# Kernel tuning notes

Measured on AMD Instinct MI355X. Metric: run time of the kernel, lower is better.

Reference implementation:

```python
import jax, jax.numpy as jnp
import numpy as np

B, N, E, H, DIN, DB, P, L, NB = 2, 10000, 100000, 128, 8, 16, 3, 2, 3


def setup_inputs() -> dict:
    key = jax.random.key(0)
    ks = jax.random.split(key, 16)

    def rn(i, shape, s=0.05):
        return jax.random.normal(ks[i], shape, dtype=jnp.float32) * s

    return {
        "x": jax.random.normal(ks[0], (B, DIN), dtype=jnp.float32),
        "base_features": rn(1, (N, DB), 1.0),
        "base_positions": rn(2, (N, P), 1.0),
        "Win": rn(3, (DB + DIN, H)),
        "b_in": jnp.zeros((H,), jnp.float32),
        "msg_W1": rn(4, (L, NB, 2 * H + 1, H)),
        "msg_b1": jnp.zeros((L, NB, H), jnp.float32),
        "msg_W2": rn(5, (L, NB, H, H)),
        "msg_b2": jnp.zeros((L, NB, H), jnp.float32),
        "pos_W1": rn(6, (L, NB, H, H)),
        "pos_b1": jnp.zeros((L, NB, H), jnp.float32),
        "pos_W2": rn(7, (L, NB, H, 1)),
        "pos_b2": jnp.zeros((L, NB, 1), jnp.float32),
        "upd_W1": rn(8, (L, 2 * H, H)),
        "upd_b1": jnp.zeros((L, H), jnp.float32),
        "upd_W2": rn(9, (L, H, H)),
        "upd_b2": jnp.zeros((L, H), jnp.float32),
        "out_W1": rn(10, (H, H)),
        "out_b1": jnp.zeros((H,), jnp.float32),
        "out_W2": rn(11, (H, 1)),
        "out_b2": jnp.zeros((1,), jnp.float32),
        "entity_indices": jax.random.randint(ks[12], (B,), 0, N),
        "edge_src": jax.random.randint(ks[13], (NB, E), 0, N),
        "edge_dst": jax.random.randint(ks[14], (NB, E), 0, N),
    }


def reference(x, base_features, base_positions, Win, b_in,
              msg_W1, msg_b1, msg_W2, msg_b2,
              pos_W1, pos_b1, pos_W2, pos_b2,
              upd_W1, upd_b1, upd_W2, upd_b2,
              out_W1, out_b1, out_W2, out_b2,
              entity_indices, edge_src, edge_dst):
    silu = jax.nn.silu
    b = x.shape[0]
    n = base_features.shape[0]
    # scatter each batch element's dynamic features onto its entity cell
    dynamic = jnp.zeros((b, n, x.shape[1]), x.dtype).at[jnp.arange(b), entity_indices].set(x)
    base = jnp.broadcast_to(base_features[None], (b, n, base_features.shape[1]))
    h = jnp.concatenate([base, dynamic], axis=-1) @ Win + b_in          # [B,N,H]
    p = jnp.broadcast_to(base_positions[None], (b, n, base_positions.shape[1]))  # [B,N,3]
    n_layers, n_nbhd = msg_W1.shape[0], edge_src.shape[0]
    for l in range(n_layers):
        m_sum = jnp.zeros_like(h)
        p_new = p
        for k in range(n_nbhd):
            src, dst = edge_src[k], edge_dst[k]
            # degree of aggregation target (matches torch bincount over indices[1])
            deg = jnp.clip(jnp.zeros((n,), h.dtype).at[dst].add(1.0), 1.0)[None, :, None]
            rel = p[:, dst] - p[:, src]                                  # [B,E,3]
            d2 = jnp.sum(rel * rel, axis=-1, keepdims=True)              # [B,E,1]
            m = silu(jnp.concatenate([h[:, dst], h[:, src], d2], axis=-1) @ msg_W1[l, k] + msg_b1[l, k])
            m = silu(m @ msg_W2[l, k] + msg_b2[l, k])                    # [B,E,H]
            m_sum = m_sum + jnp.zeros_like(h).at[:, dst].add(m) / deg
            coef = silu(m @ pos_W1[l, k] + pos_b1[l, k]) @ pos_W2[l, k] + pos_b2[l, k]  # [B,E,1]
            p_new = p_new + jnp.zeros_like(p).at[:, dst].add(rel * coef) / deg
        h = h + (silu(jnp.concatenate([h, m_sum], axis=-1) @ upd_W1[l] + upd_b1[l]) @ upd_W2[l] + upd_b2[l])
        p = p_new
    e = h[jnp.arange(b), entity_indices]                                 # [B,H] gather readout
    return silu(e @ out_W1 + out_b1) @ out_W2 + out_b2                   # [B,1]
```

## Files before the change

kernel.cpp:

```cpp
#include <hip/hip_runtime.h>
#include <hip/hip_bf16.h>
#include <math.h>

#define Bc   2
#define Nc   10000
#define Ec   100000
#define Hc   128
#define DINc 8
#define DBc  16
#define NBc  3
#define Lc   2
#define EB   3125

typedef float v4 __attribute__((ext_vector_type(4)));
typedef float f32x16 __attribute__((ext_vector_type(16)));
typedef _Float16 h8 __attribute__((ext_vector_type(8)));
typedef _Float16 h4 __attribute__((ext_vector_type(4)));

__device__ __forceinline__ float silu_f(float x) {
  return x * __builtin_amdgcn_rcpf(1.f + __expf(-x));
}

__device__ __forceinline__ h4 pack4(float a, float b, float c, float d) {
  typedef decltype(__builtin_amdgcn_cvt_pkrtz(0.f, 0.f)) pk2;
  union { h4 v; pk2 p[2]; } u;
  u.p[0] = __builtin_amdgcn_cvt_pkrtz(a, b);
  u.p[1] = __builtin_amdgcn_cvt_pkrtz(c, d);
  return u.v;
}


__global__ void zero4_kernel(float* __restrict__ p, int n4) {
  int i = blockIdx.x * blockDim.x + threadIdx.x;
  if (i < n4) ((v4*)p)[i] = (v4)(0.f);
}

__global__ void copy_kernel(float* __restrict__ dst, const float* __restrict__ src, int n) {
  int i = blockIdx.x * blockDim.x + threadIdx.x;
  if (i < n) dst[i] = src[i];
}


__global__ void hist_kernel(int* __restrict__ hist, const int* __restrict__ edst) {
  int i = blockIdx.x * blockDim.x + threadIdx.x;
  if (i < NBc * Ec) {
    int k = i / Ec;
    atomicAdd(&hist[k * Nc + edst[i]], 1);
  }
}

__global__ void scan_kernel(const int* __restrict__ hist, int* __restrict__ offs,
                            float* __restrict__ deginv) {
  const int k = blockIdx.x, tid = threadIdx.x;
  const int NPT = 40;
  __shared__ int part[256];
  int local[NPT];
  int sum = 0;
  for (int j = 0; j < NPT; ++j) {
    int n = tid * NPT + j;
    if (n < Nc) { local[j] = sum; sum += hist[k * Nc + n]; }
  }
  part[tid] = sum;
  __syncthreads();
  for (int off = 1; off < 256; off <<= 1) {
    int v = (tid >= off) ? part[tid - off] : 0;
    __syncthreads();
    part[tid] += v;
    __syncthreads();
  }
  int excl = part[tid] - sum;
  for (int j = 0; j < NPT; ++j) {
    int n = tid * NPT + j;
    if (n < Nc) {
      offs[k * Nc + n] = excl + local[j];
      deginv[k * Nc + n] = 1.f / fmaxf((float)hist[k * Nc + n], 1.f);
    }
  }
}

__global__ void sort_scatter_kernel(int* __restrict__ sorted, int* __restrict__ cursor,
                                    const int* __restrict__ offs, const int* __restrict__ edst) {
  int i = blockIdx.x * blockDim.x + threadIdx.x;
  if (i < NBc * Ec) {
    int k = i / Ec, e = i - k * Ec;
    int d = edst[i];
    int pos = offs[k * Nc + d] + atomicAdd(&cursor[k * Nc + d], 1);
    sorted[k * Ec + pos] = e;
  }
}


__global__ void init_h_kernel(_Float16* __restrict__ h16, const float* __restrict__ bfeat,
                              const float* __restrict__ x, const float* __restrict__ Win,
                              const float* __restrict__ b_in, const int* __restrict__ ent) {
  int g = blockIdx.x * blockDim.x + threadIdx.x;
  if (g >= Bc * Nc * Hc) return;
  int j = g & (Hc - 1);
  int bn = g >> 7;
  int n = bn % Nc;
  int b = bn / Nc;
  float acc = b_in[j];
#pragma unroll
  for (int i = 0; i < DBc; ++i) acc = fmaf(bfeat[n * DBc + i], Win[i * Hc + j], acc);
  if (n == ent[b]) {
#pragma unroll
    for (int i = 0; i < DINc; ++i) acc = fmaf(x[b * DINc + i], Win[(DBc + i) * Hc + j], acc);
  }
  h16[g] = (_Float16)acc;
}

__global__ void init_p_kernel(float* __restrict__ p, const float* __restrict__ bp) {
  int i = blockIdx.x * blockDim.x + threadIdx.x;
  if (i < Bc * Nc * 3) p[i] = bp[i % (Nc * 3)];
}

__global__ void conv_ext_kernel(_Float16* __restrict__ dst, const float* __restrict__ src,
                                const float* __restrict__ bias,
                                int nchunk, int total, int realRows, int biasRow) {
  int g = blockIdx.x * blockDim.x + threadIdx.x;
  if (g >= total) return;
  int j = g & 7;
  int lane = (g >> 3) & 63;
  int q = g >> 9;
  int t = q % nchunk;
  int q2 = q / nchunk;
  int wave = q2 & 3;
  int mat = q2 >> 2;
  int kk = t * 16 + (lane >> 5) * 8 + j;
  int col = (wave << 5) + (lane & 31);
  float v = 0.f;
  if (kk < realRows)      v = src[((size_t)mat * realRows + kk) * Hc + col];
  else if (kk == biasRow) v = bias[mat * Hc + col];
  dst[g] = (_Float16)v;
}


__global__ __launch_bounds__(256, 8)
void edge_mfma_kernel(const _Float16* __restrict__ h16, const float* __restrict__ p,
                      float* __restrict__ m_sum, float* __restrict__ p_new,
                      const float* __restrict__ deginv,
                      const int* __restrict__ esrc, const int* __restrict__ edst,
                      const int* __restrict__ sorted,
                      const _Float16* __restrict__ W1e, const _Float16* __restrict__ W2e,
                      const _Float16* __restrict__ P1e,
                      const float* __restrict__ pW2, const float* __restrict__ pb2,
                      int l) {
  const int k = blockIdx.y, lk = l * NBc + k;
  const int b = (blockIdx.x >= EB) ? 1 : 0;
  const int pos0 = (blockIdx.x - b * EB) << 5;
  const int tid = threadIdx.x;
  const int wave = tid >> 6, lane = tid & 63;
  const int lrow = lane & 31, lhalf = lane >> 5;

  __shared__ __align__(16) _Float16 RegA[16 * 512];
  __shared__ __align__(16) _Float16 Dchk[512];
  __shared__ int shd[32], shs[32], sdi[32];
  __shared__ float sdinvs[32], srel[32][3], scoef[32];
  __shared__ float cpw2[Hc];
  __shared__ unsigned sflush;

  if (tid < Hc) cpw2[tid] = pW2[lk * Hc + tid];
  if (tid < 32) {
    int e = sorted[k * Ec + pos0 + tid];
    int si = esrc[k * Ec + e], di = edst[k * Ec + e];
    int nd = b * Nc + di, ns = b * Nc + si;
    const float* pd = &p[(size_t)nd * 3];
    const float* ps = &p[(size_t)ns * 3];
    float rx = pd[0] - ps[0], ry = pd[1] - ps[1], rz = pd[2] - ps[2];
    srel[tid][0] = rx; srel[tid][1] = ry; srel[tid][2] = rz;
    float d2 = rx * rx + ry * ry + rz * rz;
    sdinvs[tid] = deginv[k * Nc + di];
    sdi[tid] = di;
    shd[tid] = nd * Hc; shs[tid] = ns * Hc;
    scoef[tid] = 0.f;
    h8 dv = (h8)(_Float16)0.f;
    dv[0] = (_Float16)d2; dv[1] = (_Float16)1.f;
    *(h8*)&Dchk[tid * 8] = dv;
    int prev = __shfl_up(di, 1);
    bool isStart = (tid == 0) || (di != prev);
    unsigned long long m = __ballot(isStart);
    if (tid == 0) sflush = (unsigned)((m >> 1) | 0x80000000ull);
  } else if (tid < 64) {
    h8 dv = (h8)(_Float16)0.f;
    *(h8*)&Dchk[tid * 8] = dv;
  }
  __syncthreads();

  {
    const int i = tid & 31, c = tid >> 5;
    h8 v0 = *(const h8*)&h16[shd[i] + c * 8];
    h8 v1 = *(const h8*)&h16[shd[i] + 64 + c * 8];
    h8 v2 = *(const h8*)&h16[shs[i] + c * 8];
    h8 v3 = *(const h8*)&h16[shs[i] + 64 + c * 8];
    int slot = (i + ((c & 1) << 5)) << 3;
    int tb = (c >> 1) << 9;
    *(h8*)&RegA[tb + 0 * 2048 + slot] = v0;
    *(h8*)&RegA[tb + 4 * 512  + slot] = v1;
    *(h8*)&RegA[tb + 8 * 512  + slot] = v2;
    *(h8*)&RegA[tb + 12 * 512 + slot] = v3;
  }
  __syncthreads();

  const _Float16* wb1 = &W1e[(size_t)(lk * 4 + wave) * (17 * 512)];
  f32x16 acc;
#pragma unroll
  for (int r = 0; r < 16; ++r) acc[r] = 0.f;
#pragma unroll
  for (int t = 0; t < 16; ++t) {
    h8 bact = *(const h8*)&RegA[t * 512 + lane * 8];
    h8 aw   = *(const h8*)&wb1[t * 512 + lane * 8];
    acc = __builtin_amdgcn_mfma_f32_32x32x16_f16(aw, bact, acc, 0, 0, 0);
  }
  {
    h8 bact = *(const h8*)&Dchk[lane * 8];
    h8 aw   = *(const h8*)&wb1[16 * 512 + lane * 8];
    acc = __builtin_amdgcn_mfma_f32_32x32x16_f16(aw, bact, acc, 0, 0, 0);
  }
  h4 m1pk[4];
#pragma unroll
  for (int c = 0; c < 4; ++c)
    m1pk[c] = pack4(silu_f(acc[c * 4 + 0]), silu_f(acc[c * 4 + 1]),
                    silu_f(acc[c * 4 + 2]), silu_f(acc[c * 4 + 3]));
  __syncthreads();
#pragma unroll
  for (int c = 0; c < 4; ++c) {
    int t = (wave << 1) + (c >> 1);
    int slot = lrow + ((c & 1) << 5);
    *(h4*)&RegA[t * 512 + slot * 8 + lhalf * 4] = m1pk[c];
  }
  __syncthreads();

  const _Float16* wb2 = &W2e[(size_t)(lk * 4 + wave) * (9 * 512)];
  f32x16 acc2;
#pragma unroll
  for (int r = 0; r < 16; ++r) acc2[r] = 0.f;
#pragma unroll
  for (int t = 0; t < 8; ++t) {
    h8 bact = *(const h8*)&RegA[t * 512 + lane * 8];
    h8 aw   = *(const h8*)&wb2[t * 512 + lane * 8];
    acc2 = __builtin_amdgcn_mfma_f32_32x32x16_f16(aw, bact, acc2, 0, 0, 0);
  }
  {
    h8 bact = *(const h8*)&Dchk[lane * 8];
    h8 aw   = *(const h8*)&wb2[8 * 512 + lane * 8];
    acc2 = __builtin_amdgcn_mfma_f32_32x32x16_f16(aw, bact, acc2, 0, 0, 0);
  }
  h4 m2pk[4];
#pragma unroll
  for (int c = 0; c < 4; ++c) {
    m2pk[c] = pack4(silu_f(acc2[c * 4 + 0]), silu_f(acc2[c * 4 + 1]),
                    silu_f(acc2[c * 4 + 2]), silu_f(acc2[c * 4 + 3]));
    int t = 8 + (wave << 1) + (c >> 1);
    int slot = lrow + ((c & 1) << 5);
    *(h4*)&RegA[t * 512 + slot * 8 + lhalf * 4] = m2pk[c];
  }
  __syncthreads();
  {
    char* rm = (char*)RegA;
#pragma unroll
    for (int c = 0; c < 4; ++c) {
      int hb = (wave << 5) + (c << 3) + (lhalf << 2);
      *(h4*)(rm + (lrow << 8) + (((hb << 1)) ^ ((lrow & 15) << 4))) = m2pk[c];
    }
  }

  const _Float16* wb3 = &P1e[(size_t)(lk * 4 + wave) * (9 * 512)];
  f32x16 acc3;
#pragma unroll
  for (int r = 0; r < 16; ++r) acc3[r] = 0.f;
#pragma unroll
  for (int t = 0; t < 8; ++t) {
    h8 bact = *(const h8*)&RegA[(8 + t) * 512 + lane * 8];
    h8 aw   = *(const h8*)&wb3[t * 512 + lane * 8];
    acc3 = __builtin_amdgcn_mfma_f32_32x32x16_f16(aw, bact, acc3, 0, 0, 0);
  }
  {
    h8 bact = *(const h8*)&Dchk[lane * 8];
    h8 aw   = *(const h8*)&wb3[8 * 512 + lane * 8];
    acc3 = __builtin_amdgcn_mfma_f32_32x32x16_f16(aw, bact, acc3, 0, 0, 0);
  }
  {
    float csum = 0.f;
#pragma unroll
    for (int r = 0; r < 16; ++r) {
      int hg = (wave << 5) + (r & 3) + ((r >> 2) << 3) + (lhalf << 2);
      csum += silu_f(acc3[r]) * cpw2[hg];
    }
    csum += __shfl_down(csum, 32);
    if (lane < 32) atomicAdd(&scoef[lrow], csum);
  }
  __syncthreads();

  {
    const int col = tid & 127;
    const int r0 = (tid >> 7) << 4;
    const size_t bbase = (size_t)b * Nc * Hc;
    const unsigned fm = sflush;
    const char* rm = (const char*)RegA;
    float accv = 0.f;
#pragma unroll
    for (int rr = 0; rr < 16; ++rr) {
      int r = r0 + rr;
      float v = (float)*(const _Float16*)(rm + (r << 8) + (((col << 1)) ^ ((r & 15) << 4)));
      accv += v;
      if ((fm >> r) & 1u) {
        atomicAdd(&m_sum[bbase + (size_t)sdi[r] * Hc + col], accv * sdinvs[r]);
        accv = 0.f;
      }
    }
    if (r0 == 0 && !((fm >> 15) & 1u))
      atomicAdd(&m_sum[bbase + (size_t)sdi[15] * Hc + col], accv * sdinvs[15]);
  }
  if (tid < 32) {
    float cf = (scoef[tid] + pb2[lk]) * sdinvs[tid];
    float* pp = &p_new[((size_t)(b * Nc + sdi[tid])) * 3];
    atomicAdd(&pp[0], srel[tid][0] * cf);
    atomicAdd(&pp[1], srel[tid][1] * cf);
    atomicAdd(&pp[2], srel[tid][2] * cf);
  }
}


__global__ __launch_bounds__(256, 8)
void update_mfma_kernel(_Float16* __restrict__ h16, const float* __restrict__ m_sum,
                        const _Float16* __restrict__ U1e, const _Float16* __restrict__ U2e,
                        int l) {
  const int tid = threadIdx.x;
  const int wave = tid >> 6, lane = tid & 63;
  const int lrow = lane & 31, lhalf = lane >> 5;
  const int row0 = blockIdx.x << 5;

  __shared__ __align__(16) _Float16 RegA[16 * 512];
  __shared__ __align__(16) _Float16 Dchk[512];

  if (tid < 64) {
    h8 dv = (h8)(_Float16)0.f;
    if (tid < 32) dv[1] = (_Float16)1.f;
    *(h8*)&Dchk[tid * 8] = dv;
  }
  {
    const int i = tid & 31, c = tid >> 5;
    size_t hb = (size_t)(row0 + i) * Hc;
    h8 v0 = *(const h8*)&h16[hb + c * 8];
    h8 v1 = *(const h8*)&h16[hb + 64 + c * 8];
    v4 m0 = *(const v4*)&m_sum[hb + c * 8];
    v4 m1 = *(const v4*)&m_sum[hb + c * 8 + 4];
    v4 m2 = *(const v4*)&m_sum[hb + 64 + c * 8];
    v4 m3 = *(const v4*)&m_sum[hb + 64 + c * 8 + 4];
    union { h8 v; h4 q[2]; } w0, w1;
    w0.q[0] = pack4(m0[0], m0[1], m0[2], m0[3]);
    w0.q[1] = pack4(m1[0], m1[1], m1[2], m1[3]);
    w1.q[0] = pack4(m2[0], m2[1], m2[2], m2[3]);
    w1.q[1] = pack4(m3[0], m3[1], m3[2], m3[3]);
    int slot = (i + ((c & 1) << 5)) << 3;
    int tb = (c >> 1) << 9;
    *(h8*)&RegA[tb + slot] = v0;
    *(h8*)&RegA[tb + 4 * 512 + slot] = v1;
    *(h8*)&RegA[tb + 8 * 512 + slot] = w0.v;
    *(h8*)&RegA[tb + 12 * 512 + slot] = w1.v;
  }
  __syncthreads();

  const _Float16* wb1 = &U1e[(size_t)(l * 4 + wave) * (17 * 512)];
  f32x16 acc;
#pragma unroll
  for (int r = 0; r < 16; ++r) acc[r] = 0.f;
#pragma unroll
  for (int t = 0; t < 16; ++t) {
    h8 bact = *(const h8*)&RegA[t * 512 + lane * 8];
    h8 aw   = *(const h8*)&wb1[t * 512 + lane * 8];
    acc = __builtin_amdgcn_mfma_f32_32x32x16_f16(aw, bact, acc, 0, 0, 0);
  }
  {
    h8 bact = *(const h8*)&Dchk[lane * 8];
    h8 aw   = *(const h8*)&wb1[16 * 512 + lane * 8];
    acc = __builtin_amdgcn_mfma_f32_32x32x16_f16(aw, bact, acc, 0, 0, 0);
  }
  h4 u1pk[4];
#pragma unroll
  for (int c = 0; c < 4; ++c)
    u1pk[c] = pack4(silu_f(acc[c * 4 + 0]), silu_f(acc[c * 4 + 1]),
                    silu_f(acc[c * 4 + 2]), silu_f(acc[c * 4 + 3]));
  __syncthreads();
#pragma unroll
  for (int c = 0; c < 4; ++c) {
    int t = (wave << 1) + (c >> 1);
    int slot = lrow + ((c & 1) << 5);
    *(h4*)&RegA[t * 512 + slot * 8 + lhalf * 4] = u1pk[c];
  }
  __syncthreads();

  const _Float16* wb2 = &U2e[(size_t)(l * 4 + wave) * (9 * 512)];
  f32x16 acc2;
#pragma unroll
  for (int r = 0; r < 16; ++r) acc2[r] = 0.f;
#pragma unroll
  for (int t = 0; t < 8; ++t) {
    h8 bact = *(const h8*)&RegA[t * 512 + lane * 8];
    h8 aw   = *(const h8*)&wb2[t * 512 + lane * 8];
    acc2 = __builtin_amdgcn_mfma_f32_32x32x16_f16(aw, bact, acc2, 0, 0, 0);
  }
  {
    h8 bact = *(const h8*)&Dchk[lane * 8];
    h8 aw   = *(const h8*)&wb2[8 * 512 + lane * 8];
    acc2 = __builtin_amdgcn_mfma_f32_32x32x16_f16(aw, bact, acc2, 0, 0, 0);
  }
  {
    _Float16* hp = &h16[(size_t)(row0 + lrow) * Hc];
#pragma unroll
    for (int c = 0; c < 4; ++c) {
      int hb = (wave << 5) + (c << 3) + (lhalf << 2);
      h4 old = *(const h4*)&hp[hb];
      *(h4*)&hp[hb] = pack4((float)old[0] + acc2[c * 4 + 0], (float)old[1] + acc2[c * 4 + 1],
                            (float)old[2] + acc2[c * 4 + 2], (float)old[3] + acc2[c * 4 + 3]);
    }
  }
}


__global__ void readout_kernel(const _Float16* __restrict__ h16, const int* __restrict__ ent,
                               const float* __restrict__ oW1, const float* __restrict__ ob1,
                               const float* __restrict__ oW2, const float* __restrict__ ob2,
                               float* __restrict__ out) {
  __shared__ float tb[Bc][Hc];
  int tid = threadIdx.x;
  int b = tid >> 7, j = tid & 127;
  const _Float16* e = &h16[((size_t)(b * Nc + ent[b])) * Hc];
  float a = ob1[j];
#pragma unroll 4
  for (int i = 0; i < Hc; ++i) a = fmaf((float)e[i], oW1[i * Hc + j], a);
  tb[b][j] = silu_f(a);
  __syncthreads();
  if (tid < Bc) {
    float s = ob2[0];
    for (int i = 0; i < Hc; ++i) s = fmaf(tb[tid][i], oW2[i], s);
    out[tid] = s;
  }
}


extern "C" void kernel_launch(void* const* d_in, const int* in_sizes, int n_in,
                              void* d_out, int out_size, void* d_ws, size_t ws_size,
                              hipStream_t stream) {
  const float* x    = (const float*)d_in[0];
  const float* bfe  = (const float*)d_in[1];
  const float* bp   = (const float*)d_in[2];
  const float* Win  = (const float*)d_in[3];
  const float* b_in = (const float*)d_in[4];
  const float* mW1  = (const float*)d_in[5];
  const float* mb1  = (const float*)d_in[6];
  const float* mW2  = (const float*)d_in[7];
  const float* mb2  = (const float*)d_in[8];
  const float* pW1  = (const float*)d_in[9];
  const float* pb1  = (const float*)d_in[10];
  const float* pW2  = (const float*)d_in[11];
  const float* pb2  = (const float*)d_in[12];
  const float* uW1  = (const float*)d_in[13];
  const float* ub1  = (const float*)d_in[14];
  const float* uW2  = (const float*)d_in[15];
  const float* ub2  = (const float*)d_in[16];
  const float* oW1  = (const float*)d_in[17];
  const float* ob1  = (const float*)d_in[18];
  const float* oW2  = (const float*)d_in[19];
  const float* ob2  = (const float*)d_in[20];
  const int* ent    = (const int*)d_in[21];
  const int* esrc   = (const int*)d_in[22];
  const int* edst   = (const int*)d_in[23];

  float* wsf = (float*)d_ws;
  float* msum   = wsf;  wsf += (size_t)Bc * Nc * Hc;
  float* pa     = wsf;  wsf += (size_t)Bc * Nc * 3;
  float* pb_    = wsf;  wsf += (size_t)Bc * Nc * 3;
  float* deginv = wsf;  wsf += (size_t)NBc * Nc;
  _Float16* h16 = (_Float16*)wsf;
  _Float16* W1e = h16 + (size_t)Bc * Nc * Hc;
  _Float16* W2e = W1e + 208896;
  _Float16* P1e = W2e + 110592;
  _Float16* U1e = P1e + 110592;
  _Float16* U2e = U1e + 69632;
  int* hist   = (int*)(U2e + 36864);
  int* cursor = hist + NBc * Nc;
  int* offs   = cursor + NBc * Nc;
  int* sorted = offs + NBc * Nc;

  zero4_kernel<<<dim3((2 * NBc * Nc / 4 + 255) / 256), dim3(256), 0, stream>>>((float*)hist, 2 * NBc * Nc / 4);
  hist_kernel<<<dim3((NBc * Ec + 255) / 256), dim3(256), 0, stream>>>(hist, edst);
  scan_kernel<<<dim3(NBc), dim3(256), 0, stream>>>(hist, offs, deginv);
  sort_scatter_kernel<<<dim3((NBc * Ec + 255) / 256), dim3(256), 0, stream>>>(sorted, cursor, offs, edst);

  conv_ext_kernel<<<dim3(816), dim3(256), 0, stream>>>(W1e, mW1, mb1, 17, 208896, 257, 257);
  conv_ext_kernel<<<dim3(432), dim3(256), 0, stream>>>(W2e, mW2, mb2, 9, 110592, 128, 129);
  conv_ext_kernel<<<dim3(432), dim3(256), 0, stream>>>(P1e, pW1, pb1, 9, 110592, 128, 129);
  conv_ext_kernel<<<dim3(272), dim3(256), 0, stream>>>(U1e, uW1, ub1, 17, 69632, 256, 257);
  conv_ext_kernel<<<dim3(144), dim3(256), 0, stream>>>(U2e, uW2, ub2, 9, 36864, 128, 129);

  init_h_kernel<<<dim3((Bc * Nc * Hc + 255) / 256), dim3(256), 0, stream>>>(h16, bfe, x, Win, b_in, ent);
  init_p_kernel<<<dim3((Bc * Nc * 3 + 255) / 256), dim3(256), 0, stream>>>(pa, bp);

  float* pcur = pa;
  float* pnew = pb_;
  const int nmh = Bc * Nc * Hc;
  for (int l = 0; l < Lc; ++l) {
    zero4_kernel<<<dim3((nmh / 4 + 255) / 256), dim3(256), 0, stream>>>(msum, nmh / 4);
    copy_kernel<<<dim3((Bc * Nc * 3 + 255) / 256), dim3(256), 0, stream>>>(pnew, pcur, Bc * Nc * 3);
    edge_mfma_kernel<<<dim3(Bc * EB, NBc), dim3(256), 0, stream>>>(
        h16, pcur, msum, pnew, deginv, esrc, edst, sorted,
        W1e, W2e, P1e, pW2, pb2, l);
    update_mfma_kernel<<<dim3(Bc * Nc / 32), dim3(256), 0, stream>>>(h16, msum, U1e, U2e, l);
    float* t = pcur; pcur = pnew; pnew = t;
  }
  readout_kernel<<<dim3(1), dim3(256), 0, stream>>>(h16, ent, oW1, ob1, oW2, ob2, (float*)d_out);
}
```

Before: 672.1 us.

## Process 64 edges per block, reusing each weight fragment across two MFMAs

The edge kernel now handles 64 sorted edges per block instead of 32, split into two 32-edge column groups that share each loaded weight fragment across two MFMA calls. This halves the weight reads from global memory per edge and halves the block count. The cost is double the LDS use and more registers per thread (launch bounds lowered to 4 blocks per CU). The m_sum scatter now reads the second-layer output straight from the regular tile layout instead of a separate swizzled copy, and flush detection uses a 64-bit mask keyed on the batch-offset node.

New measurement: 669.6 us. About the same (-0.4%).

```diff
diff --git a/kernel.cpp b/kernel.cpp
--- a/kernel.cpp
+++ b/kernel.cpp
@@ -10,7 +10,6 @@
 #define DBc  16
 #define NBc  3
 #define Lc   2
-#define EB   3125
 
 typedef float v4 __attribute__((ext_vector_type(4)));
 typedef float f32x16 __attribute__((ext_vector_type(16)));
@@ -135,7 +134,7 @@
 }
 
 
-__global__ __launch_bounds__(256, 8)
+__global__ __launch_bounds__(256, 4)
 void edge_mfma_kernel(const _Float16* __restrict__ h16, const float* __restrict__ p,
                       float* __restrict__ m_sum, float* __restrict__ p_new,
                       const float* __restrict__ deginv,
@@ -146,22 +145,22 @@
                       const float* __restrict__ pW2, const float* __restrict__ pb2,
                       int l) {
   const int k = blockIdx.y, lk = l * NBc + k;
-  const int b = (blockIdx.x >= EB) ? 1 : 0;
-  const int pos0 = (blockIdx.x - b * EB) << 5;
   const int tid = threadIdx.x;
   const int wave = tid >> 6, lane = tid & 63;
   const int lrow = lane & 31, lhalf = lane >> 5;
 
-  __shared__ __align__(16) _Float16 RegA[16 * 512];
-  __shared__ __align__(16) _Float16 Dchk[512];
-  __shared__ int shd[32], shs[32], sdi[32];
-  __shared__ float sdinvs[32], srel[32][3], scoef[32];
+  __shared__ __align__(16) _Float16 RegA[16384];
+  __shared__ __align__(16) _Float16 Dchk[1024];
+  __shared__ int shd[64], shs[64], sOff[64];
+  __shared__ float sdinv[64], srel[64][3], scoef[64];
   __shared__ float cpw2[Hc];
-  __shared__ unsigned sflush;
+  __shared__ unsigned long long sflush;
 
   if (tid < Hc) cpw2[tid] = pW2[lk * Hc + tid];
-  if (tid < 32) {
-    int e = sorted[k * Ec + pos0 + tid];
+  if (tid < 64) {
+    int pos = blockIdx.x * 64 + tid;
+    int b = (pos >= Ec) ? 1 : 0;
+    int e = sorted[k * Ec + (pos - b * Ec)];
     int si = esrc[k * Ec + e], di = edst[k * Ec + e];
     int nd = b * Nc + di, ns = b * Nc + si;
     const float* pd = &p[(size_t)nd * 3];
@@ -169,151 +168,163 @@
     float rx = pd[0] - ps[0], ry = pd[1] - ps[1], rz = pd[2] - ps[2];
     srel[tid][0] = rx; srel[tid][1] = ry; srel[tid][2] = rz;
     float d2 = rx * rx + ry * ry + rz * rz;
-    sdinvs[tid] = deginv[k * Nc + di];
-    sdi[tid] = di;
+    sdinv[tid] = deginv[k * Nc + di];
     shd[tid] = nd * Hc; shs[tid] = ns * Hc;
+    sOff[tid] = nd * Hc;
     scoef[tid] = 0.f;
     h8 dv = (h8)(_Float16)0.f;
+    h8 zv = (h8)(_Float16)0.f;
     dv[0] = (_Float16)d2; dv[1] = (_Float16)1.f;
-    *(h8*)&Dchk[tid * 8] = dv;
-    int prev = __shfl_up(di, 1);
-    bool isStart = (tid == 0) || (di != prev);
+    int g = tid >> 5, il = tid & 31;
+    *(h8*)&Dchk[g * 512 + il * 8] = dv;
+    *(h8*)&Dchk[g * 512 + 256 + il * 8] = zv;
+    int prevn = __shfl_up(nd, 1);
+    bool isStart = (tid == 0) || (nd != prevn);
     unsigned long long m = __ballot(isStart);
-    if (tid == 0) sflush = (unsigned)((m >> 1) | 0x80000000ull);
-  } else if (tid < 64) {
-    h8 dv = (h8)(_Float16)0.f;
-    *(h8*)&Dchk[tid * 8] = dv;
-  }
-  __syncthreads();
-
-  {
-    const int i = tid & 31, c = tid >> 5;
-    h8 v0 = *(const h8*)&h16[shd[i] + c * 8];
-    h8 v1 = *(const h8*)&h16[shd[i] + 64 + c * 8];
-    h8 v2 = *(const h8*)&h16[shs[i] + c * 8];
-    h8 v3 = *(const h8*)&h16[shs[i] + 64 + c * 8];
-    int slot = (i + ((c & 1) << 5)) << 3;
-    int tb = (c >> 1) << 9;
-    *(h8*)&RegA[tb + 0 * 2048 + slot] = v0;
-    *(h8*)&RegA[tb + 4 * 512  + slot] = v1;
-    *(h8*)&RegA[tb + 8 * 512  + slot] = v2;
-    *(h8*)&RegA[tb + 12 * 512 + slot] = v3;
+    if (tid == 0) sflush = (m >> 1) | (1ull << 63);
+  }
+  __syncthreads();
+
+  {
+    const int i = tid & 63, cg = tid >> 6;
+    const int g = i >> 5, il = i & 31;
+#pragma unroll
+    for (int q = 0; q < 4; ++q) {
+      int d0 = cg * 32 + q * 8;
+      int t = d0 >> 4;
+      int kh = q & 1;
+      h8 vd = *(const h8*)&h16[shd[i] + d0];
+      h8 vs = *(const h8*)&h16[shs[i] + d0];
+      *(h8*)&RegA[(t * 2 + g) * 512 + kh * 256 + il * 8] = vd;
+      *(h8*)&RegA[((8 + t) * 2 + g) * 512 + kh * 256 + il * 8] = vs;
+    }
   }
   __syncthreads();
 
   const _Float16* wb1 = &W1e[(size_t)(lk * 4 + wave) * (17 * 512)];
-  f32x16 acc;
-#pragma unroll
-  for (int r = 0; r < 16; ++r) acc[r] = 0.f;
+  f32x16 aA, aB;
+#pragma unroll
+  for (int r = 0; r < 16; ++r) { aA[r] = 0.f; aB[r] = 0.f; }
 #pragma unroll
   for (int t = 0; t < 16; ++t) {
-    h8 bact = *(const h8*)&RegA[t * 512 + lane * 8];
-    h8 aw   = *(const h8*)&wb1[t * 512 + lane * 8];
-    acc = __builtin_amdgcn_mfma_f32_32x32x16_f16(aw, bact, acc, 0, 0, 0);
-  }
-  {
-    h8 bact = *(const h8*)&Dchk[lane * 8];
-    h8 aw   = *(const h8*)&wb1[16 * 512 + lane * 8];
-    acc = __builtin_amdgcn_mfma_f32_32x32x16_f16(aw, bact, acc, 0, 0, 0);
-  }
-  h4 m1pk[4];
-#pragma unroll
-  for (int c = 0; c < 4; ++c)
-    m1pk[c] = pack4(silu_f(acc[c * 4 + 0]), silu_f(acc[c * 4 + 1]),
-                    silu_f(acc[c * 4 + 2]), silu_f(acc[c * 4 + 3]));
-  __syncthreads();
+    h8 aw = *(const h8*)&wb1[t * 512 + lane * 8];
+    h8 bA = *(const h8*)&RegA[(t * 2 + 0) * 512 + lane * 8];
+    h8 bB = *(const h8*)&RegA[(t * 2 + 1) * 512 + lane * 8];
+    aA = __builtin_amdgcn_mfma_f32_32x32x16_f16(aw, bA, aA, 0, 0, 0);
+    aB = __builtin_amdgcn_mfma_f32_32x32x16_f16(aw, bB, aB, 0, 0, 0);
+  }
+  {
+    h8 aw = *(const h8*)&wb1[16 * 512 + lane * 8];
+    h8 dA = *(const h8*)&Dchk[lane * 8];
+    h8 dB = *(const h8*)&Dchk[512 + lane * 8];
+    aA = __builtin_amdgcn_mfma_f32_32x32x16_f16(aw, dA, aA, 0, 0, 0);
+    aB = __builtin_amdgcn_mfma_f32_32x32x16_f16(aw, dB, aB, 0, 0, 0);
+  }
+  h4 m1A[4], m1B[4];
 #pragma unroll
   for (int c = 0; c < 4; ++c) {
-    int t = (wave << 1) + (c >> 1);
-    int slot = lrow + ((c & 1) << 5);
-    *(h4*)&RegA[t * 512 + slot * 8 + lhalf * 4] = m1pk[c];
+    m1A[c] = pack4(silu_f(aA[c * 4 + 0]), silu_f(aA[c * 4 + 1]),
+                   silu_f(aA[c * 4 + 2]), silu_f(aA[c * 4 + 3]));
+    m1B[c] = pack4(silu_f(aB[c * 4 + 0]), silu_f(aB[c * 4 + 1]),
+                   silu_f(aB[c * 4 + 2]), silu_f(aB[c * 4 + 3]));
+  }
+  __syncthreads();
+#pragma unroll
+  for (int c = 0; c < 4; ++c) {
+    int t = 2 * wave + (c >> 1);
+    int base = (c & 1) * 256 + lrow * 8 + lhalf * 4;
+    *(h4*)&RegA[(t * 2 + 0) * 512 + base] = m1A[c];
+    *(h4*)&RegA[(t * 2 + 1) * 512 + base] = m1B[c];
   }
   __syncthreads();
 
   const _Float16* wb2 = &W2e[(size_t)(lk * 4 + wave) * (9 * 512)];
-  f32x16 acc2;
-#pragma unroll
-  for (int r = 0; r < 16; ++r) acc2[r] = 0.f;
+#pragma unroll
+  for (int r = 0; r < 16; ++r) { aA[r] = 0.f; aB[r] = 0.f; }
 #pragma unroll
   for (int t = 0; t < 8; ++t) {
-    h8 bact = *(const h8*)&RegA[t * 512 + lane * 8];
-    h8 aw   = *(const h8*)&wb2[t * 512 + lane * 8];
-    acc2 = __builtin_amdgcn_mfma_f32_32x32x16_f16(aw, bact, acc2, 0, 0, 0);
-  }
-  {
-    h8 bact = *(const h8*)&Dchk[lane * 8];
-    h8 aw   = *(const h8*)&wb2[8 * 512 + lane * 8];
-    acc2 = __builtin_amdgcn_mfma_f32_32x32x16_f16(aw, bact, acc2, 0, 0, 0);
-  }
-  h4 m2pk[4];
+    h8 aw = *(const h8*)&wb2[t * 512 + lane * 8];
+    h8 bA = *(const h8*)&RegA[(t * 2 + 0) * 512 + lane * 8];
+    h8 bB = *(const h8*)&RegA[(t * 2 + 1) * 512 + lane * 8];
+    aA = __builtin_amdgcn_mfma_f32_32x32x16_f16(aw, bA, aA, 0, 0, 0);
+    aB = __builtin_amdgcn_mfma_f32_32x32x16_f16(aw, bB, aB, 0, 0, 0);
+  }
+  {
+    h8 aw = *(const h8*)&wb2[8 * 512 + lane * 8];
+    h8 dA = *(const h8*)&Dchk[lane * 8];
+    h8 dB = *(const h8*)&Dchk[512 + lane * 8];
+    aA = __builtin_amdgcn_mfma_f32_32x32x16_f16(aw, dA, aA, 0, 0, 0);
+    aB = __builtin_amdgcn_mfma_f32_32x32x16_f16(aw, dB, aB, 0, 0, 0);
+  }
 #pragma unroll
   for (int c = 0; c < 4; ++c) {
-    m2pk[c] = pack4(silu_f(acc2[c * 4 + 0]), silu_f(acc2[c * 4 + 1]),
-                    silu_f(acc2[c * 4 + 2]), silu_f(acc2[c * 4 + 3]));
-    int t = 8 + (wave << 1) + (c >> 1);
-    int slot = lrow + ((c & 1) << 5);
-    *(h4*)&RegA[t * 512 + slot * 8 + lhalf * 4] = m2pk[c];
-  }
-  __syncthreads();
-  {
-    char* rm = (char*)RegA;
-#pragma unroll
-    for (int c = 0; c < 4; ++c) {
-      int hb = (wave << 5) + (c << 3) + (lhalf << 2);
-      *(h4*)(rm + (lrow << 8) + (((hb << 1)) ^ ((lrow & 15) << 4))) = m2pk[c];
-    }
-  }
+    h4 p2A = pack4(silu_f(aA[c * 4 + 0]), silu_f(aA[c * 4 + 1]),
+                   silu_f(aA[c * 4 + 2]), silu_f(aA[c * 4 + 3]));
+    h4 p2B = pack4(silu_f(aB[c * 4 + 0]), silu_f(aB[c * 4 + 1]),
+                   silu_f(aB[c * 4 + 2]), silu_f(aB[c * 4 + 3]));
+    int t2 = 8 + 2 * wave + (c >> 1);
+    int base = (c & 1) * 256 + lrow * 8 + lhalf * 4;
+    *(h4*)&RegA[(t2 * 2 + 0) * 512 + base] = p2A;
+    *(h4*)&RegA[(t2 * 2 + 1) * 512 + base] = p2B;
+  }
+  __syncthreads();
 
   const _Float16* wb3 = &P1e[(size_t)(lk * 4 + wave) * (9 * 512)];
-  f32x16 acc3;
-#pragma unroll
-  for (int r = 0; r < 16; ++r) acc3[r] = 0.f;
+#pragma unroll
+  for (int r = 0; r < 16; ++r) { aA[r] = 0.f; aB[r] = 0.f; }
 #pragma unroll
   for (int t = 0; t < 8; ++t) {
-    h8 bact = *(const h8*)&RegA[(8 + t) * 512 + lane * 8];
-    h8 aw   = *(const h8*)&wb3[t * 512 + lane * 8];
-    acc3 = __builtin_amdgcn_mfma_f32_32x32x16_f16(aw, bact, acc3, 0, 0, 0);
-  }
-  {
-    h8 bact = *(const h8*)&Dchk[lane * 8];
-    h8 aw   = *(const h8*)&wb3[8 * 512 + lane * 8];
-    acc3 = __builtin_amdgcn_mfma_f32_32x32x16_f16(aw, bact, acc3, 0, 0, 0);
-  }
-  {
-    float csum = 0.f;
+    h8 aw = *(const h8*)&wb3[t * 512 + lane * 8];
+    h8 bA = *(const h8*)&RegA[((8 + t) * 2 + 0) * 512 + lane * 8];
+    h8 bB = *(const h8*)&RegA[((8 + t) * 2 + 1) * 512 + lane * 8];
+    aA = __builtin_amdgcn_mfma_f32_32x32x16_f16(aw, bA, aA, 0, 0, 0);
+    aB = __builtin_amdgcn_mfma_f32_32x32x16_f16(aw, bB, aB, 0, 0, 0);
+  }
+  {
+    h8 aw = *(const h8*)&wb3[8 * 512 + lane * 8];
+    h8 dA = *(const h8*)&Dchk[lane * 8];
+    h8 dB = *(const h8*)&Dchk[512 + lane * 8];
+    aA = __builtin_amdgcn_mfma_f32_32x32x16_f16(aw, dA, aA, 0, 0, 0);
+    aB = __builtin_amdgcn_mfma_f32_32x32x16_f16(aw, dB, aB, 0, 0, 0);
+  }
+  {
+    float csA = 0.f, csB = 0.f;
 #pragma unroll
     for (int r = 0; r < 16; ++r) {
       int hg = (wave << 5) + (r & 3) + ((r >> 2) << 3) + (lhalf << 2);
-      csum += silu_f(acc3[r]) * cpw2[hg];
+      csA += silu_f(aA[r]) * cpw2[hg];
+      csB += silu_f(aB[r]) * cpw2[hg];
     }
-    csum += __shfl_down(csum, 32);
-    if (lane < 32) atomicAdd(&scoef[lrow], csum);
-  }
-  __syncthreads();
+    csA += __shfl_down(csA, 32);
+    csB += __shfl_down(csB, 32);
+    if (lane < 32) {
+      atomicAdd(&scoef[lrow], csA);
+      atomicAdd(&scoef[32 + lrow], csB);
+    }
+  }
 
   {
     const int col = tid & 127;
-    const int r0 = (tid >> 7) << 4;
-    const size_t bbase = (size_t)b * Nc * Hc;
-    const unsigned fm = sflush;
-    const char* rm = (const char*)RegA;
+    const int half = tid >> 7;
+    const int base = ((8 + (col >> 4)) * 2 + half) * 512 + ((col >> 3) & 1) * 256 + (col & 7);
+    const unsigned long long fm = sflush;
     float accv = 0.f;
 #pragma unroll
-    for (int rr = 0; rr < 16; ++rr) {
-      int r = r0 + rr;
-      float v = (float)*(const _Float16*)(rm + (r << 8) + (((col << 1)) ^ ((r & 15) << 4)));
-      accv += v;
-      if ((fm >> r) & 1u) {
-        atomicAdd(&m_sum[bbase + (size_t)sdi[r] * Hc + col], accv * sdinvs[r]);
+    for (int rr = 0; rr < 32; ++rr) {
+      int r = half * 32 + rr;
+      accv += (float)RegA[base + rr * 8];
+      if ((fm >> r) & 1ull) {
+        atomicAdd(&m_sum[sOff[r] + col], accv * sdinv[r]);
         accv = 0.f;
       }
     }
-    if (r0 == 0 && !((fm >> 15) & 1u))
-      atomicAdd(&m_sum[bbase + (size_t)sdi[15] * Hc + col], accv * sdinvs[15]);
-  }
-  if (tid < 32) {
-    float cf = (scoef[tid] + pb2[lk]) * sdinvs[tid];
-    float* pp = &p_new[((size_t)(b * Nc + sdi[tid])) * 3];
+    if (half == 0 && !((fm >> 31) & 1ull))
+      atomicAdd(&m_sum[sOff[31] + col], accv * sdinv[31]);
+  }
+  __syncthreads();
+  if (tid < 64) {
+    float cf = (scoef[tid] + pb2[lk]) * sdinv[tid];
+    float* pp = &p_new[(size_t)(sOff[tid] / Hc) * 3];
     atomicAdd(&pp[0], srel[tid][0] * cf);
     atomicAdd(&pp[1], srel[tid][1] * cf);
     atomicAdd(&pp[2], srel[tid][2] * cf);
@@ -503,7 +514,7 @@
   for (int l = 0; l < Lc; ++l) {
     zero4_kernel<<<dim3((nmh / 4 + 255) / 256), dim3(256), 0, stream>>>(msum, nmh / 4);
     copy_kernel<<<dim3((Bc * Nc * 3 + 255) / 256), dim3(256), 0, stream>>>(pnew, pcur, Bc * Nc * 3);
-    edge_mfma_kernel<<<dim3(Bc * EB, NBc), dim3(256), 0, stream>>>(
+    edge_mfma_kernel<<<dim3(Bc * Ec / 64, NBc), dim3(256), 0, stream>>>(
         h16, pcur, msum, pnew, deginv, esrc, edst, sorted,
         W1e, W2e, P1e, pW2, pb2, l);
     update_mfma_kernel<<<dim3(Bc * Nc / 32), dim3(256), 0, stream>>>(h16, msum, U1e, U2e, l);
```

## Make edge kernel persistent with per-wave MFMA weights held in registers

Applied to the files above, without the earlier changes.

Turns the edge kernel into a grid-stride persistent kernel: 1250 blocks per neighborhood each loop over 32-edge groups instead of launching one block per group. Each wave loads its slices of the W1, W2 and P1 weights into registers once and reuses them for every group, so the per-group global weight reloads go away. The cost is about 35 h8 weight registers per lane, so launch bounds drop from 8 to 4 blocks per CU, which lowers occupancy and leaves less latency hiding for the h16 gathers and atomics. Group indexing now covers both batches through a linear position, and the flush detection compares node ids that include the batch offset.

New measurement: 1.232 ms. +83.2%, slower.

```diff
diff --git a/kernel.cpp b/kernel.cpp
--- a/kernel.cpp
+++ b/kernel.cpp
@@ -10,7 +10,8 @@
 #define DBc  16
 #define NBc  3
 #define Lc   2
-#define EB   3125
+#define GRPS 6250
+#define PBLK 1250
 
 typedef float v4 __attribute__((ext_vector_type(4)));
 typedef float f32x16 __attribute__((ext_vector_type(16)));
@@ -135,7 +136,7 @@
 }
 
 
-__global__ __launch_bounds__(256, 8)
+__global__ __launch_bounds__(256, 4)
 void edge_mfma_kernel(const _Float16* __restrict__ h16, const float* __restrict__ p,
                       float* __restrict__ m_sum, float* __restrict__ p_new,
                       const float* __restrict__ deginv,
@@ -146,177 +147,177 @@
                       const float* __restrict__ pW2, const float* __restrict__ pb2,
                       int l) {
   const int k = blockIdx.y, lk = l * NBc + k;
-  const int b = (blockIdx.x >= EB) ? 1 : 0;
-  const int pos0 = (blockIdx.x - b * EB) << 5;
   const int tid = threadIdx.x;
   const int wave = tid >> 6, lane = tid & 63;
   const int lrow = lane & 31, lhalf = lane >> 5;
 
   __shared__ __align__(16) _Float16 RegA[16 * 512];
   __shared__ __align__(16) _Float16 Dchk[512];
-  __shared__ int shd[32], shs[32], sdi[32];
+  __shared__ int shd[32], shs[32], snd[32];
   __shared__ float sdinvs[32], srel[32][3], scoef[32];
   __shared__ float cpw2[Hc];
   __shared__ unsigned sflush;
 
+  const _Float16* wb1 = &W1e[(size_t)(lk * 4 + wave) * (17 * 512)];
+  const _Float16* wb2 = &W2e[(size_t)(lk * 4 + wave) * (9 * 512)];
+  const _Float16* wb3 = &P1e[(size_t)(lk * 4 + wave) * (9 * 512)];
+  h8 w1r[17], w2r[9], w3r[9];
+#pragma unroll
+  for (int t = 0; t < 17; ++t) w1r[t] = *(const h8*)&wb1[t * 512 + lane * 8];
+#pragma unroll
+  for (int t = 0; t < 9; ++t)  w2r[t] = *(const h8*)&wb2[t * 512 + lane * 8];
+#pragma unroll
+  for (int t = 0; t < 9; ++t)  w3r[t] = *(const h8*)&wb3[t * 512 + lane * 8];
+
   if (tid < Hc) cpw2[tid] = pW2[lk * Hc + tid];
-  if (tid < 32) {
-    int e = sorted[k * Ec + pos0 + tid];
-    int si = esrc[k * Ec + e], di = edst[k * Ec + e];
-    int nd = b * Nc + di, ns = b * Nc + si;
-    const float* pd = &p[(size_t)nd * 3];
-    const float* ps = &p[(size_t)ns * 3];
-    float rx = pd[0] - ps[0], ry = pd[1] - ps[1], rz = pd[2] - ps[2];
-    srel[tid][0] = rx; srel[tid][1] = ry; srel[tid][2] = rz;
-    float d2 = rx * rx + ry * ry + rz * rz;
-    sdinvs[tid] = deginv[k * Nc + di];
-    sdi[tid] = di;
-    shd[tid] = nd * Hc; shs[tid] = ns * Hc;
-    scoef[tid] = 0.f;
-    h8 dv = (h8)(_Float16)0.f;
-    dv[0] = (_Float16)d2; dv[1] = (_Float16)1.f;
-    *(h8*)&Dchk[tid * 8] = dv;
-    int prev = __shfl_up(di, 1);
-    bool isStart = (tid == 0) || (di != prev);
-    unsigned long long m = __ballot(isStart);
-    if (tid == 0) sflush = (unsigned)((m >> 1) | 0x80000000ull);
-  } else if (tid < 64) {
-    h8 dv = (h8)(_Float16)0.f;
-    *(h8*)&Dchk[tid * 8] = dv;
-  }
-  __syncthreads();
-
-  {
-    const int i = tid & 31, c = tid >> 5;
-    h8 v0 = *(const h8*)&h16[shd[i] + c * 8];
-    h8 v1 = *(const h8*)&h16[shd[i] + 64 + c * 8];
-    h8 v2 = *(const h8*)&h16[shs[i] + c * 8];
-    h8 v3 = *(const h8*)&h16[shs[i] + 64 + c * 8];
-    int slot = (i + ((c & 1) << 5)) << 3;
-    int tb = (c >> 1) << 9;
-    *(h8*)&RegA[tb + 0 * 2048 + slot] = v0;
-    *(h8*)&RegA[tb + 4 * 512  + slot] = v1;
-    *(h8*)&RegA[tb + 8 * 512  + slot] = v2;
-    *(h8*)&RegA[tb + 12 * 512 + slot] = v3;
-  }
-  __syncthreads();
-
-  const _Float16* wb1 = &W1e[(size_t)(lk * 4 + wave) * (17 * 512)];
-  f32x16 acc;
-#pragma unroll
-  for (int r = 0; r < 16; ++r) acc[r] = 0.f;
-#pragma unroll
-  for (int t = 0; t < 16; ++t) {
-    h8 bact = *(const h8*)&RegA[t * 512 + lane * 8];
-    h8 aw   = *(const h8*)&wb1[t * 512 + lane * 8];
-    acc = __builtin_amdgcn_mfma_f32_32x32x16_f16(aw, bact, acc, 0, 0, 0);
-  }
-  {
-    h8 bact = *(const h8*)&Dchk[lane * 8];
-    h8 aw   = *(const h8*)&wb1[16 * 512 + lane * 8];
-    acc = __builtin_amdgcn_mfma_f32_32x32x16_f16(aw, bact, acc, 0, 0, 0);
-  }
-  h4 m1pk[4];
-#pragma unroll
-  for (int c = 0; c < 4; ++c)
-    m1pk[c] = pack4(silu_f(acc[c * 4 + 0]), silu_f(acc[c * 4 + 1]),
-                    silu_f(acc[c * 4 + 2]), silu_f(acc[c * 4 + 3]));
-  __syncthreads();
-#pragma unroll
-  for (int c = 0; c < 4; ++c) {
-    int t = (wave << 1) + (c >> 1);
-    int slot = lrow + ((c & 1) << 5);
-    *(h4*)&RegA[t * 512 + slot * 8 + lhalf * 4] = m1pk[c];
-  }
-  __syncthreads();
-
-  const _Float16* wb2 = &W2e[(size_t)(lk * 4 + wave) * (9 * 512)];
-  f32x16 acc2;
-#pragma unroll
-  for (int r = 0; r < 16; ++r) acc2[r] = 0.f;
-#pragma unroll
-  for (int t = 0; t < 8; ++t) {
-    h8 bact = *(const h8*)&RegA[t * 512 + lane * 8];
-    h8 aw   = *(const h8*)&wb2[t * 512 + lane * 8];
-    acc2 = __builtin_amdgcn_mfma_f32_32x32x16_f16(aw, bact, acc2, 0, 0, 0);
-  }
-  {
-    h8 bact = *(const h8*)&Dchk[lane * 8];
-    h8 aw   = *(const h8*)&wb2[8 * 512 + lane * 8];
-    acc2 = __builtin_amdgcn_mfma_f32_32x32x16_f16(aw, bact, acc2, 0, 0, 0);
-  }
-  h4 m2pk[4];
-#pragma unroll
-  for (int c = 0; c < 4; ++c) {
-    m2pk[c] = pack4(silu_f(acc2[c * 4 + 0]), silu_f(acc2[c * 4 + 1]),
-                    silu_f(acc2[c * 4 + 2]), silu_f(acc2[c * 4 + 3]));
-    int t = 8 + (wave << 1) + (c >> 1);
-    int slot = lrow + ((c & 1) << 5);
-    *(h4*)&RegA[t * 512 + slot * 8 + lhalf * 4] = m2pk[c];
-  }
-  __syncthreads();
-  {
-    char* rm = (char*)RegA;
+  if (tid >= 32 && tid < 64) {
+    h8 zv = (h8)(_Float16)0.f;
+    *(h8*)&Dchk[tid * 8] = zv;
+  }
+  const float pb2v = pb2[lk];
+
+  for (int grp = blockIdx.x; grp < GRPS; grp += PBLK) {
+    __syncthreads();
+    if (tid < 32) {
+      int pos = grp * 32 + tid;
+      int b = (pos >= Ec) ? 1 : 0;
+      int e = sorted[k * Ec + (pos - b * Ec)];
+      int si = esrc[k * Ec + e], di = edst[k * Ec + e];
+      int nd = b * Nc + di, ns = b * Nc + si;
+      const float* pd = &p[(size_t)nd * 3];
+      const float* ps = &p[(size_t)ns * 3];
+      float rx = pd[0] - ps[0], ry = pd[1] - ps[1], rz = pd[2] - ps[2];
+      srel[tid][0] = rx; srel[tid][1] = ry; srel[tid][2] = rz;
+      float d2 = rx * rx + ry * ry + rz * rz;
+      sdinvs[tid] = deginv[k * Nc + di];
+      snd[tid] = nd;
+      shd[tid] = nd * Hc; shs[tid] = ns * Hc;
+      scoef[tid] = 0.f;
+      h8 dv = (h8)(_Float16)0.f;
+      dv[0] = (_Float16)d2; dv[1] = (_Float16)1.f;
+      *(h8*)&Dchk[tid * 8] = dv;
+      int prev = __shfl_up(nd, 1);
+      bool isStart = (tid == 0) || (nd != prev);
+      unsigned long long m = __ballot(isStart);
+      if (tid == 0) sflush = (unsigned)((m >> 1) | 0x80000000ull);
+    }
+    __syncthreads();
+
+    {
+      const int i = tid & 31, c = tid >> 5;
+      h8 v0 = *(const h8*)&h16[shd[i] + c * 8];
+      h8 v1 = *(const h8*)&h16[shd[i] + 64 + c * 8];
+      h8 v2 = *(const h8*)&h16[shs[i] + c * 8];
+      h8 v3 = *(const h8*)&h16[shs[i] + 64 + c * 8];
+      int slot = (i + ((c & 1) << 5)) << 3;
+      int tb = (c >> 1) << 9;
+      *(h8*)&RegA[tb + slot] = v0;
+      *(h8*)&RegA[tb + 4 * 512 + slot] = v1;
+      *(h8*)&RegA[tb + 8 * 512 + slot] = v2;
+      *(h8*)&RegA[tb + 12 * 512 + slot] = v3;
+    }
+    __syncthreads();
+
+    h8 dR = *(const h8*)&Dchk[lane * 8];
+
+    f32x16 acc;
+#pragma unroll
+    for (int r = 0; r < 16; ++r) acc[r] = 0.f;
+#pragma unroll
+    for (int t = 0; t < 16; ++t) {
+      h8 bact = *(const h8*)&RegA[t * 512 + lane * 8];
+      acc = __builtin_amdgcn_mfma_f32_32x32x16_f16(w1r[t], bact, acc, 0, 0, 0);
+    }
+    acc = __builtin_amdgcn_mfma_f32_32x32x16_f16(w1r[16], dR, acc, 0, 0, 0);
+    h4 m1pk[4];
+#pragma unroll
+    for (int c = 0; c < 4; ++c)
+      m1pk[c] = pack4(silu_f(acc[c * 4 + 0]), silu_f(acc[c * 4 + 1]),
+                      silu_f(acc[c * 4 + 2]), silu_f(acc[c * 4 + 3]));
+    __syncthreads();
 #pragma unroll
     for (int c = 0; c < 4; ++c) {
-      int hb = (wave << 5) + (c << 3) + (lhalf << 2);
-      *(h4*)(rm + (lrow << 8) + (((hb << 1)) ^ ((lrow & 15) << 4))) = m2pk[c];
-    }
-  }
-
-  const _Float16* wb3 = &P1e[(size_t)(lk * 4 + wave) * (9 * 512)];
-  f32x16 acc3;
-#pragma unroll
-  for (int r = 0; r < 16; ++r) acc3[r] = 0.f;
-#pragma unroll
-  for (int t = 0; t < 8; ++t) {
-    h8 bact = *(const h8*)&RegA[(8 + t) * 512 + lane * 8];
-    h8 aw   = *(const h8*)&wb3[t * 512 + lane * 8];
-    acc3 = __builtin_amdgcn_mfma_f32_32x32x16_f16(aw, bact, acc3, 0, 0, 0);
-  }
-  {
-    h8 bact = *(const h8*)&Dchk[lane * 8];
-    h8 aw   = *(const h8*)&wb3[8 * 512 + lane * 8];
-    acc3 = __builtin_amdgcn_mfma_f32_32x32x16_f16(aw, bact, acc3, 0, 0, 0);
-  }
-  {
-    float csum = 0.f;
-#pragma unroll
-    for (int r = 0; r < 16; ++r) {
-      int hg = (wave << 5) + (r & 3) + ((r >> 2) << 3) + (lhalf << 2);
-      csum += silu_f(acc3[r]) * cpw2[hg];
-    }
-    csum += __shfl_down(csum, 32);
-    if (lane < 32) atomicAdd(&scoef[lrow], csum);
-  }
-  __syncthreads();
-
-  {
-    const int col = tid & 127;
-    const int r0 = (tid >> 7) << 4;
-    const size_t bbase = (size_t)b * Nc * Hc;
-    const unsigned fm = sflush;
-    const char* rm = (const char*)RegA;
-    float accv = 0.f;
-#pragma unroll
-    for (int rr = 0; rr < 16; ++rr) {
-      int r = r0 + rr;
-      float v = (float)*(const _Float16*)(rm + (r << 8) + (((col << 1)) ^ ((r & 15) << 4)));
-      accv += v;
-      if ((fm >> r) & 1u) {
-        atomicAdd(&m_sum[bbase + (size_t)sdi[r] * Hc + col], accv * sdinvs[r]);
-        accv = 0.f;
+      int t = (wave << 1) + (c >> 1);
+      int slot = lrow + ((c & 1) << 5);
+      *(h4*)&RegA[t * 512 + slot * 8 + lhalf * 4] = m1pk[c];
+    }
+    __syncthreads();
+
+    f32x16 acc2;
+#pragma unroll
+    for (int r = 0; r < 16; ++r) acc2[r] = 0.f;
+#pragma unroll
+    for (int t = 0; t < 8; ++t) {
+      h8 bact = *(const h8*)&RegA[t * 512 + lane * 8];
+      acc2 = __builtin_amdgcn_mfma_f32_32x32x16_f16(w2r[t], bact, acc2, 0, 0, 0);
+    }
+    acc2 = __builtin_amdgcn_mfma_f32_32x32x16_f16(w2r[8], dR, acc2, 0, 0, 0);
+    h4 m2pk[4];
+#pragma unroll
+    for (int c = 0; c < 4; ++c) {
+      m2pk[c] = pack4(silu_f(acc2[c * 4 + 0]), silu_f(acc2[c * 4 + 1]),
+                      silu_f(acc2[c * 4 + 2]), silu_f(acc2[c * 4 + 3]));
+      int t = 8 + (wave << 1) + (c >> 1);
+      int slot = lrow + ((c & 1) << 5);
+      *(h4*)&RegA[t * 512 + slot * 8 + lhalf * 4] = m2pk[c];
+    }
+    __syncthreads();
+    {
+      char* rm = (char*)RegA;
+#pragma unroll
+      for (int c = 0; c < 4; ++c) {
+        int hb = (wave << 5) + (c << 3) + (lhalf << 2);
+        *(h4*)(rm + (lrow << 8) + (((hb << 1)) ^ ((lrow & 15) << 4))) = m2pk[c];
       }
     }
-    if (r0 == 0 && !((fm >> 15) & 1u))
-      atomicAdd(&m_sum[bbase + (size_t)sdi[15] * Hc + col], accv * sdinvs[15]);
-  }
-  if (tid < 32) {
-    float cf = (scoef[tid] + pb2[lk]) * sdinvs[tid];
-    float* pp = &p_new[((size_t)(b * Nc + sdi[tid])) * 3];
-    atomicAdd(&pp[0], srel[tid][0] * cf);
-    atomicAdd(&pp[1], srel[tid][1] * cf);
-    atomicAdd(&pp[2], srel[tid][2] * cf);
+
+    f32x16 acc3;
+#pragma unroll
+    for (int r = 0; r < 16; ++r) acc3[r] = 0.f;
+#pragma unroll
+    for (int t = 0; t < 8; ++t) {
+      h8 bact = *(const h8*)&RegA[(8 + t) * 512 + lane * 8];
+      acc3 = __builtin_amdgcn_mfma_f32_32x32x16_f16(w3r[t], bact, acc3, 0, 0, 0);
+    }
+    acc3 = __builtin_amdgcn_mfma_f32_32x32x16_f16(w3r[8], dR, acc3, 0, 0, 0);
+    {
+      float csum = 0.f;
+#pragma unroll
+      for (int r = 0; r < 16; ++r) {
+        int hg = (wave << 5) + (r & 3) + ((r >> 2) << 3) + (lhalf << 2);
+        csum += silu_f(acc3[r]) * cpw2[hg];
+      }
+      csum += __shfl_down(csum, 32);
+      if (lane < 32) atomicAdd(&scoef[lrow], csum);
+    }
+    __syncthreads();
+
+    {
+      const int col = tid & 127;
+      const int r0 = (tid >> 7) << 4;
+      const unsigned fm = sflush;
+      const char* rm = (const char*)RegA;
+      float accv = 0.f;
+#pragma unroll
+      for (int rr = 0; rr < 16; ++rr) {
+        int r = r0 + rr;
+        float v = (float)*(const _Float16*)(rm + (r << 8) + (((col << 1)) ^ ((r & 15) << 4)));
+        accv += v;
+        if ((fm >> r) & 1u) {
+          atomicAdd(&m_sum[snd[r] * Hc + col], accv * sdinvs[r]);
+          accv = 0.f;
+        }
+      }
+      if (r0 == 0 && !((fm >> 15) & 1u))
+        atomicAdd(&m_sum[snd[15] * Hc + col], accv * sdinvs[15]);
+    }
+    if (tid < 32) {
+      float cf = (scoef[tid] + pb2v) * sdinvs[tid];
+      float* pp = &p_new[(size_t)snd[tid] * 3];
+      atomicAdd(&pp[0], srel[tid][0] * cf);
+      atomicAdd(&pp[1], srel[tid][1] * cf);
+      atomicAdd(&pp[2], srel[tid][2] * cf);
+    }
   }
 }
 
@@ -503,7 +504,7 @@
   for (int l = 0; l < Lc; ++l) {
     zero4_kernel<<<dim3((nmh / 4 + 255) / 256), dim3(256), 0, stream>>>(msum, nmh / 4);
     copy_kernel<<<dim3((Bc * Nc * 3 + 255) / 256), dim3(256), 0, stream>>>(pnew, pcur, Bc * Nc * 3);
-    edge_mfma_kernel<<<dim3(Bc * EB, NBc), dim3(256), 0, stream>>>(
+    edge_mfma_kernel<<<dim3(PBLK, NBc), dim3(256), 0, stream>>>(
         h16, pcur, msum, pnew, deginv, esrc, edst, sorted,
         W1e, W2e, P1e, pW2, pb2, l);
     update_mfma_kernel<<<dim3(Bc * Nc / 32), dim3(256), 0, stream>>>(h16, msum, U1e, U2e, l);
```
